# Kernel optimization log

Measured on AMD Instinct MI355X. Metric: run time of the kernel, lower is better.

Reference implementation:

```python
import jax, jax.numpy as jnp
import numpy as np

B, S, T = 4096, 512, 32


def setup_inputs() -> dict:
    key = jax.random.key(0)
    k1, k2, k3, k4, k5 = jax.random.split(key, 5)
    emissions = jax.random.normal(k1, (B, S, T), dtype=jnp.float32)
    tags = jax.random.randint(k2, (B, S), 0, T)
    mask = jnp.ones((B, S), dtype=bool)
    transitions = jax.random.normal(k3, (T, T), dtype=jnp.float32)
    start_transitions = jax.random.normal(k4, (T,), dtype=jnp.float32)
    end_transitions = jax.random.normal(k5, (T,), dtype=jnp.float32)
    return {
        "emissions": emissions,
        "tags": tags,
        "mask": mask,
        "transitions": transitions,
        "start_transitions": start_transitions,
        "end_transitions": end_transitions,
    }


def _score_sentence(emissions, tags, mask, transitions, start_transitions, end_transitions):
    # gold path score, fully vectorized over batch and time
    t0 = tags[:, 0]
    score = start_transitions[t0]
    score = score + jnp.take_along_axis(emissions[:, 0], t0[:, None], axis=1)[:, 0]
    maskf = mask[:, 1:].astype(emissions.dtype)  # [B, S-1]
    trans_sc = transitions[tags[:, :-1], tags[:, 1:]]  # [B, S-1]
    emit_sc = jnp.take_along_axis(emissions[:, 1:], tags[:, 1:, None], axis=2)[..., 0]
    score = score + ((trans_sc + emit_sc) * maskf).sum(axis=1)
    last_idx = mask.sum(axis=1).astype(jnp.int32) - 1  # [B]
    last_tags = jnp.take_along_axis(tags, last_idx[:, None], axis=1)[:, 0]
    score = score + end_transitions[last_tags]
    return score  # [B]


def _forward_algorithm(emissions, mask, transitions, start_transitions, end_transitions):
    # log partition via lax.scan over time; state is [B, T]
    score0 = start_transitions + emissions[:, 0]  # [B, T]
    em_rest = jnp.swapaxes(emissions[:, 1:], 0, 1)  # [S-1, B, T]
    mk_rest = jnp.swapaxes(mask[:, 1:], 0, 1)  # [S-1, B]

    def step(score, xs):
        em_i, m_i = xs
        # score[b,prev] + transitions[prev,next] + em_i[b,next]
        next_score = jax.nn.logsumexp(
            score[:, :, None] + transitions[None, :, :] + em_i[:, None, :], axis=1
        )
        score = jnp.where(m_i[:, None], next_score, score)
        return score, None

    score, _ = jax.lax.scan(step, score0, (em_rest, mk_rest))
    return jax.nn.logsumexp(score + end_transitions, axis=1)  # [B]


def reference(emissions, tags, mask, transitions, start_transitions, end_transitions):
    gold = _score_sentence(emissions, tags, mask, transitions, start_transitions, end_transitions)
    fwd = _forward_algorithm(emissions, mask, transitions, start_transitions, end_transitions)
    return (fwd - gold).mean()
```

## Files before the change

### kernel.cpp

```cpp
#include <hip/hip_runtime.h>
#include <hip/hip_bf16.h>


#define L2E 1.4426950408889634f
#define LN2 0.6931471805599453f
#define PD  16

typedef float v2f __attribute__((ext_vector_type(2)));

__device__ __forceinline__ float readlane_f(float v, int slane) {
    return __uint_as_float(__builtin_amdgcn_readlane(__float_as_uint(v), slane));
}
__device__ __forceinline__ float readfirst_f(float v) {
    return __uint_as_float(__builtin_amdgcn_readfirstlane(__float_as_uint(v)));
}

__global__ __launch_bounds__(256, 4) void crf_kernel(
    const float* __restrict__ emissions,
    const int*   __restrict__ tags,
    const float* __restrict__ transitions,
    const float* __restrict__ start_t,
    const float* __restrict__ end_t,
    float* __restrict__ out)
{
    constexpr int S = 512, T = 32;

    __shared__ float trans_raw[T * T];
    __shared__ __align__(16) float u_lds[4][T];
    __shared__ float res_lds[4];

    const int tid  = threadIdx.x;
    const int lane = tid & 63;
    const int tcol = lane & 31;
    const int half = lane >> 5;
    const int wv   = tid >> 6;
    const long b   = (long)blockIdx.x * 4 + wv;

    #pragma unroll
    for (int k = 0; k < 4; ++k)
        trans_raw[tid + 256 * k] = transitions[tid + 256 * k];
    __syncthreads();

    const int koff = half * 16;
    v2f vv2[8];
    #pragma unroll
    for (int j = 0; j < 8; ++j) {
        float a = __builtin_amdgcn_exp2f(transitions[(koff + 2 * j)     * T + tcol] * L2E);
        float c = __builtin_amdgcn_exp2f(transitions[(koff + 2 * j + 1) * T + tcol] * L2E);
        vv2[j] = (v2f){a, c};
    }

    const float* em_base = emissions + b * (long)(S * T) + tcol;
    const int*   tg_base = tags + b * S;

    float em0   = em_base[0];
    int   sprev = __builtin_amdgcn_readfirstlane(tg_base[0]);

    float em_buf[PD];
    int   tag_buf[PD];
    #pragma unroll
    for (int j = 0; j < PD; ++j) {
        em_buf[j]  = em_base[(long)(1 + j) * T];
        tag_buf[j] = tg_base[1 + j];
    }

    float startv  = start_t[tcol];
    float r       = (startv + em0) * L2E;
    float offs    = 0.0f;
    float bk_prev = 0.0f;
    float gold = readlane_f(startv, sprev) + readlane_f(em0, sprev);

    float* u_row = &u_lds[wv][0];
    const float4* up = reinterpret_cast<const float4*>(u_row + koff);

    auto step = [&](float em_cur, int tag_cur) {
        float u = __builtin_amdgcn_exp2f(r);
        u_row[tcol] = u;
        __builtin_amdgcn_wave_barrier();
        float4 u0 = up[0], u1 = up[1], u2 = up[2], u3 = up[3];
        __builtin_amdgcn_wave_barrier();

        v2f p0 = (v2f){u0.x, u0.y} * vv2[0];
        p0 = __builtin_elementwise_fma((v2f){u0.z, u0.w}, vv2[1], p0);
        v2f p1 = (v2f){u1.x, u1.y} * vv2[2];
        p1 = __builtin_elementwise_fma((v2f){u1.z, u1.w}, vv2[3], p1);
        v2f p2 = (v2f){u2.x, u2.y} * vv2[4];
        p2 = __builtin_elementwise_fma((v2f){u2.z, u2.w}, vv2[5], p2);
        v2f p3 = (v2f){u3.x, u3.y} * vv2[6];
        p3 = __builtin_elementwise_fma((v2f){u3.z, u3.w}, vv2[7], p3);
        v2f q = (p0 + p1) + (p2 + p3);
        float s_half = q.x + q.y;
        float s = s_half + __shfl_xor(s_half, 32, 64);

        float r_raw = fmaf(em_cur, L2E, __builtin_amdgcn_logf(s));
        r     = r_raw - bk_prev;
        offs += bk_prev;
        bk_prev = readfirst_f(r);

        int scur = __builtin_amdgcn_readfirstlane(tag_cur);
        gold += trans_raw[sprev * 32 + scur] + readlane_f(em_cur, scur);
        sprev = scur;
    };

    for (int ii = 1; ii <= 465; ii += 16) {
        const float* pf_em = em_base + (long)(ii + 16) * T;
        const int*   pf_tg = tg_base + (ii + 16);
        #pragma unroll
        for (int j = 0; j < 16; ++j) {
            float em_cur = em_buf[j];
            int   tag_cur = tag_buf[j];
            em_buf[j]  = pf_em[(long)j * T];
            tag_buf[j] = pf_tg[j];
            step(em_cur, tag_cur);
        }
    }
    {
        const float* pf_em = em_base + (long)497 * T;
        const int*   pf_tg = tg_base + 497;
        #pragma unroll
        for (int j = 0; j < 15; ++j) {
            float em_cur = em_buf[j];
            int   tag_cur = tag_buf[j];
            em_buf[j]  = pf_em[(long)j * T];
            tag_buf[j] = pf_tg[j];
            step(em_cur, tag_cur);
        }
    }
    #pragma unroll
    for (int j = 0; j < 16; ++j) {
        const int bi = (j + 15) & 15;
        step(em_buf[bi], tag_buf[bi]);
    }

    float endv = end_t[tcol];
    gold += readlane_f(endv, sprev);

    float x = r + endv * L2E;
    float m = x;
    #pragma unroll
    for (int d = 16; d >= 1; d >>= 1) m = fmaxf(m, __shfl_xor(m, d, 64));
    float e = __builtin_amdgcn_exp2f(x - m);
    #pragma unroll
    for (int d = 16; d >= 1; d >>= 1) e += __shfl_xor(e, d, 64);
    float fwd2 = offs + m + __builtin_amdgcn_logf(e);

    float resv = fwd2 * LN2 - gold;

    if (lane == 0) res_lds[wv] = resv;
    __syncthreads();
    if (tid == 0) {
        atomicAdd(out, (res_lds[0] + res_lds[1] + res_lds[2] + res_lds[3])
                       * (1.0f / 4096.0f));
    }
}

extern "C" void kernel_launch(void* const* d_in, const int* in_sizes, int n_in,
                              void* d_out, int out_size, void* d_ws, size_t ws_size,
                              hipStream_t stream) {
    const float* emissions   = (const float*)d_in[0];
    const int*   tags        = (const int*)d_in[1];
    const float* transitions = (const float*)d_in[3];
    const float* start_t     = (const float*)d_in[4];
    const float* end_t       = (const float*)d_in[5];
    float* out = (float*)d_out;

    hipMemsetAsync(out, 0, sizeof(float), stream);
    crf_kernel<<<1024, 256, 0, stream>>>(emissions, tags, transitions,
                                         start_t, end_t, out);
}
```

Measured before the change: 413.3 us.

## Run CRF forward recursion in linear domain with periodic power-of-two rescaling

Keeps the forward state as linear-domain probabilities and multiplies by exp(emission) instead of taking log then exp on every step. This removes a log and an exp from the serial dependency chain. Every fourth step the state is renormalised by a power of two built from the exponent bits of lane 0's value, and the exponent is accumulated as an integer. The trade-off is a risk of float overflow or underflow between renormalisations, plus reduced precision when lanes differ widely in magnitude.

```diff
diff --git a/kernel.cpp b/kernel.cpp
--- a/kernel.cpp
+++ b/kernel.cpp
@@ -64,18 +64,18 @@
         tag_buf[j] = tg_base[1 + j];
     }
 
-    float startv  = start_t[tcol];
-    float r       = (startv + em0) * L2E;
-    float offs    = 0.0f;
-    float bk_prev = 0.0f;
+    float startv = start_t[tcol];
+    float u_next = __builtin_amdgcn_exp2f((startv + em0) * L2E);
+    int   offs_i = 0;
     float gold = readlane_f(startv, sprev) + readlane_f(em0, sprev);
 
     float* u_row = &u_lds[wv][0];
     const float4* up = reinterpret_cast<const float4*>(u_row + koff);
 
-    auto step = [&](float em_cur, int tag_cur) {
-        float u = __builtin_amdgcn_exp2f(r);
-        u_row[tcol] = u;
+    auto step = [&](float em_cur, int tag_cur, bool rn) {
+        float E = __builtin_amdgcn_exp2f(em_cur * L2E);
+
+        u_row[tcol] = u_next;
         __builtin_amdgcn_wave_barrier();
         float4 u0 = up[0], u1 = up[1], u2 = up[2], u3 = up[3];
         __builtin_amdgcn_wave_barrier();
@@ -92,10 +92,14 @@
         float s_half = q.x + q.y;
         float s = s_half + __shfl_xor(s_half, 32, 64);
 
-        float r_raw = fmaf(em_cur, L2E, __builtin_amdgcn_logf(s));
-        r     = r_raw - bk_prev;
-        offs += bk_prev;
-        bk_prev = readfirst_f(r);
+        float un = s * E;
+        if (rn) {
+            float rf = readfirst_f(u0.x);
+            unsigned su = __float_as_uint(rf) & 0x7f800000u;
+            offs_i += (int)(su >> 23) - 127;
+            un *= __uint_as_float(0x7f000000u - su);
+        }
+        u_next = un;
 
         int scur = __builtin_amdgcn_readfirstlane(tag_cur);
         gold += trans_raw[sprev * 32 + scur] + readlane_f(em_cur, scur);
@@ -111,7 +115,7 @@
             int   tag_cur = tag_buf[j];
             em_buf[j]  = pf_em[(long)j * T];
             tag_buf[j] = pf_tg[j];
-            step(em_cur, tag_cur);
+            step(em_cur, tag_cur, (j & 3) == 3);
         }
     }
     {
@@ -123,26 +127,23 @@
             int   tag_cur = tag_buf[j];
             em_buf[j]  = pf_em[(long)j * T];
             tag_buf[j] = pf_tg[j];
-            step(em_cur, tag_cur);
+            step(em_cur, tag_cur, (j & 3) == 3);
         }
     }
     #pragma unroll
     for (int j = 0; j < 16; ++j) {
         const int bi = (j + 15) & 15;
-        step(em_buf[bi], tag_buf[bi]);
+        step(em_buf[bi], tag_buf[bi], (j & 3) == 0);
     }
 
     float endv = end_t[tcol];
     gold += readlane_f(endv, sprev);
 
-    float x = r + endv * L2E;
-    float m = x;
-    #pragma unroll
-    for (int d = 16; d >= 1; d >>= 1) m = fmaxf(m, __shfl_xor(m, d, 64));
-    float e = __builtin_amdgcn_exp2f(x - m);
+    float x = u_next * __builtin_amdgcn_exp2f(endv * L2E);
+    float e = x;
     #pragma unroll
     for (int d = 16; d >= 1; d >>= 1) e += __shfl_xor(e, d, 64);
-    float fwd2 = offs + m + __builtin_amdgcn_logf(e);
+    float fwd2 = (float)offs_i + __builtin_amdgcn_logf(e);
 
     float resv = fwd2 * LN2 - gold;
 
```

New measurement: 405.4 us. About the same (-1.9%).
